# Optimization experiments

Hardware: AMD Instinct MI355X
Metric: run time of the kernel (lower is better)

## Reference

```python
import jax, jax.numpy as jnp
import numpy as np

F = 1024
K = 32
N = 2048
EPS = 1e-6


def setup_inputs() -> dict:
    key = jax.random.key(0)
    ks = jax.random.split(key, 10)
    x = jax.random.normal(ks[0], (N, F), dtype=jnp.float32)
    idx = jax.random.randint(ks[1], (F, K), 0, F)
    norm_w = jnp.ones((F,), dtype=jnp.float32)
    w1 = jax.random.normal(ks[2], (F, K), dtype=jnp.float32) / np.sqrt(K)
    b1 = jnp.zeros((F,), dtype=jnp.float32)
    w2 = jax.random.normal(ks[3], (F, K), dtype=jnp.float32) / np.sqrt(K)
    b2 = jnp.zeros((F,), dtype=jnp.float32)
    amp = jnp.ones((F,), dtype=jnp.float32)
    freq = jnp.ones((F,), dtype=jnp.float32)
    decay = jnp.full((F,), 0.01, dtype=jnp.float32)
    alpha = jnp.ones((1,), dtype=jnp.float32)
    return {"x": x, "in_index_per_out": idx, "norm_w": norm_w,
            "w1": w1, "b1": b1, "amp": amp, "freq": freq, "decay": decay,
            "w2": w2, "b2": b2, "alpha": alpha}


def _rmsnorm(x, g):
    ms = jnp.mean(x * x, axis=-1, keepdims=True)
    return x * jax.lax.rsqrt(ms + EPS) * g


def _geo_sparse_linear(h, idx, w, b):
    hg = h[:, idx]
    return jnp.einsum('nok,ok->no', hg, w) + b


def _sine_param(z, amp, freq, decay):
    return amp * jnp.sin(freq * z) * jnp.exp(-decay * z * z)


def reference(x, in_index_per_out, norm_w, w1, b1, amp, freq, decay, w2, b2, alpha):
    h = _rmsnorm(x, norm_w)
    h = _sine_param(_geo_sparse_linear(h, in_index_per_out, w1, b1), amp, freq, decay)
    h = _geo_sparse_linear(h, in_index_per_out, w2, b2)
    return x + alpha * h
```

## Files before the change

### kernel.cpp

```cpp
#include <hip/hip_runtime.h>
#include <hip/hip_bf16.h>

#define FDIM 1024
#define KNZ 32
#define NROWS 2048
#define RB 8
#define TPB 1024
#define EPSV 1e-6f

static_assert(TPB == FDIM, "o = tid mapping requires TPB == FDIM");
static_assert(NROWS % RB == 0, "rows divide");

__device__ __forceinline__ unsigned int swz(unsigned int i) {
  return i ^ ((i >> 3) & 7u);
}

__device__ __forceinline__ unsigned int f2bf(float f) {
  unsigned int u = __float_as_uint(f);
  u += 0x7fffu + ((u >> 16) & 1u);
  return u >> 16;
}

__device__ __forceinline__ unsigned int pack2bf(float a, float b) {
  return f2bf(a) | (f2bf(b) << 16);
}

__global__ void geo_prep(const int* __restrict__ idx,
                         const float* __restrict__ w1,
                         const float* __restrict__ w2,
                         unsigned* __restrict__ pr1, unsigned* __restrict__ pr2) {
  __shared__ int   li[16 * 33];
  __shared__ float l1[16 * 33];
  __shared__ float l2[16 * 33];
  const int t = threadIdx.x;
  const int o0 = blockIdx.x * 16;
  #pragma unroll
  for (int e = 0; e < 2; ++e) {
    int j = t + e * 256;
    int ol = j >> 5, k = j & 31;
    int g = o0 * KNZ + j;
    li[ol * 33 + k] = idx[g];
    l1[ol * 33 + k] = w1[g];
    l2[ol * 33 + k] = w2[g];
  }
  __syncthreads();
  #pragma unroll
  for (int e = 0; e < 2; ++e) {
    int j = t + e * 256;
    int ol = j & 15, k = j >> 4;
    unsigned off = swz((unsigned)li[ol * 33 + k]);
    unsigned wb1 = __float_as_uint(l1[ol * 33 + k]) & 0xFFFFFC00u;
    unsigned wb2 = __float_as_uint(l2[ol * 33 + k]) & 0xFFFFFC00u;
    pr1[k * FDIM + o0 + ol] = wb1 | off;
    pr2[k * FDIM + o0 + ol] = wb2 | off;
  }
}

__device__ __forceinline__ void gather8(unsigned pw, const uint4* lds, float* acc) {
  float w = __uint_as_float(pw);
  uint4 hv = lds[pw & 1023u];
  const unsigned int* hd = reinterpret_cast<const unsigned int*>(&hv);
  #pragma unroll
  for (int d = 0; d < 4; ++d) {
    acc[2 * d]     = fmaf(__uint_as_float(hd[d] << 16), w, acc[2 * d]);
    acc[2 * d + 1] = fmaf(__uint_as_float(hd[d] & 0xffff0000u), w, acc[2 * d + 1]);
  }
}

template <bool TR>
__global__ __launch_bounds__(TPB, 4)
void geo_main(const float* __restrict__ x, const float* __restrict__ norm_w,
              const float* __restrict__ b1, const float* __restrict__ amp,
              const float* __restrict__ freq, const float* __restrict__ decay,
              const float* __restrict__ b2, const float* __restrict__ alpha,
              const unsigned* __restrict__ pr1, const unsigned* __restrict__ pr2,
              const int* __restrict__ idx, const float* __restrict__ w1,
              const float* __restrict__ w2, float* __restrict__ out) {
  __shared__ uint4 h_lds[FDIM];
  __shared__ uint4 s_lds[FDIM];
  __shared__ float red[(TPB / 64) * RB];
  __shared__ float rs_sh[RB];

  const int tid = threadIdx.x;
  const int lane = tid & 63;
  const int wid = tid >> 6;
  const int r0 = blockIdx.x * RB;
  const int o = tid;

  float v[RB];
  #pragma unroll
  for (int r = 0; r < RB; ++r)
    v[r] = x[(r0 + r) * FDIM + tid];

  const float g = norm_w[tid];

  {
    float p[RB];
    #pragma unroll
    for (int r = 0; r < RB; ++r) p[r] = v[r] * v[r];
    #pragma unroll
    for (int r = 0; r < 4; ++r) {
      float up = __shfl_xor(p[r + 4], 4, 64);
      float dn = __shfl_xor(p[r], 4, 64);
      p[r] = (lane & 4) ? (p[r + 4] + up) : (p[r] + dn);
    }
    #pragma unroll
    for (int r = 0; r < 2; ++r) {
      float up = __shfl_xor(p[r + 2], 2, 64);
      float dn = __shfl_xor(p[r], 2, 64);
      p[r] = (lane & 2) ? (p[r + 2] + up) : (p[r] + dn);
    }
    {
      float up = __shfl_xor(p[1], 1, 64);
      float dn = __shfl_xor(p[0], 1, 64);
      p[0] = (lane & 1) ? (p[1] + up) : (p[0] + dn);
    }
    p[0] += __shfl_xor(p[0], 8, 64);
    p[0] += __shfl_xor(p[0], 16, 64);
    p[0] += __shfl_xor(p[0], 32, 64);
    if (lane < RB) red[wid * RB + lane] = p[0];
  }

  {
    uint4 h;
    h.x = pack2bf(g * v[0], g * v[1]);
    h.y = pack2bf(g * v[2], g * v[3]);
    h.z = pack2bf(g * v[4], g * v[5]);
    h.w = pack2bf(g * v[6], g * v[7]);
    h_lds[swz((unsigned)tid)] = h;
  }

  __syncthreads();

  {
    float a = red[lane] + red[64 + lane];
    a += __shfl_xor(a, 8, 64);
    a += __shfl_xor(a, 16, 64);
    a += __shfl_xor(a, 32, 64);
    if (lane < RB) rs_sh[lane] = rsqrtf(a * (1.0f / FDIM) + EPSV);
  }

  float acc[RB] = {0.f, 0.f, 0.f, 0.f, 0.f, 0.f, 0.f, 0.f};

  if (TR) {
    #pragma unroll
    for (int gk = 0; gk < 4; ++gk) {
      unsigned u[8];
      #pragma unroll
      for (int j = 0; j < 8; ++j) u[j] = pr1[(gk * 8 + j) * FDIM + o];
      #pragma unroll
      for (int j = 0; j < 8; ++j) gather8(u[j], h_lds, acc);
    }
  } else {
    #pragma unroll 8
    for (int k = 0; k < KNZ; ++k) {
      unsigned off = swz((unsigned)idx[o * KNZ + k]);
      unsigned wb = __float_as_uint(w1[o * KNZ + k]) & 0xFFFFFC00u;
      gather8(wb | off, h_lds, acc);
    }
  }

  {
    const float bb1 = b1[o], am = amp[o], fq = freq[o], dc = decay[o];
    const float4 ra = *reinterpret_cast<const float4*>(&rs_sh[0]);
    const float4 rb = *reinterpret_cast<const float4*>(&rs_sh[4]);
    const float rsv[RB] = {ra.x, ra.y, ra.z, ra.w, rb.x, rb.y, rb.z, rb.w};
    float s[RB];
    #pragma unroll
    for (int r = 0; r < RB; ++r) {
      float z = fmaf(acc[r], rsv[r], bb1);
      s[r] = am * __sinf(fq * z) * __expf(-dc * z * z);
    }
    uint4 sv;
    sv.x = pack2bf(s[0], s[1]);
    sv.y = pack2bf(s[2], s[3]);
    sv.z = pack2bf(s[4], s[5]);
    sv.w = pack2bf(s[6], s[7]);
    s_lds[swz((unsigned)o)] = sv;
  }
  __syncthreads();

  #pragma unroll
  for (int r = 0; r < RB; ++r) acc[r] = 0.f;

  if (TR) {
    #pragma unroll
    for (int gk = 0; gk < 4; ++gk) {
      unsigned u[8];
      #pragma unroll
      for (int j = 0; j < 8; ++j) u[j] = pr2[(gk * 8 + j) * FDIM + o];
      #pragma unroll
      for (int j = 0; j < 8; ++j) gather8(u[j], s_lds, acc);
    }
  } else {
    #pragma unroll 8
    for (int k = 0; k < KNZ; ++k) {
      unsigned off = swz((unsigned)idx[o * KNZ + k]);
      unsigned wb = __float_as_uint(w2[o * KNZ + k]) & 0xFFFFFC00u;
      gather8(wb | off, s_lds, acc);
    }
  }

  {
    const float bb2 = b2[o];
    const float al = alpha[0];
    #pragma unroll
    for (int r = 0; r < RB; ++r)
      out[(r0 + r) * FDIM + o] = fmaf(al, acc[r] + bb2, v[r]);
  }
}

extern "C" void kernel_launch(void* const* d_in, const int* in_sizes, int n_in,
                              void* d_out, int out_size, void* d_ws, size_t ws_size,
                              hipStream_t stream) {
  const float* x      = (const float*)d_in[0];
  const int*   idx    = (const int*)d_in[1];
  const float* norm_w = (const float*)d_in[2];
  const float* w1     = (const float*)d_in[3];
  const float* b1     = (const float*)d_in[4];
  const float* amp    = (const float*)d_in[5];
  const float* freq   = (const float*)d_in[6];
  const float* decay  = (const float*)d_in[7];
  const float* w2     = (const float*)d_in[8];
  const float* b2     = (const float*)d_in[9];
  const float* alpha  = (const float*)d_in[10];
  float* out = (float*)d_out;

  const size_t need = 2ull * FDIM * KNZ * sizeof(unsigned);
  if (ws_size >= need) {
    unsigned* pr1 = (unsigned*)d_ws;
    unsigned* pr2 = pr1 + (size_t)FDIM * KNZ;
    geo_prep<<<FDIM / 16, 256, 0, stream>>>(idx, w1, w2, pr1, pr2);
    geo_main<true><<<NROWS / RB, TPB, 0, stream>>>(
        x, norm_w, b1, amp, freq, decay, b2, alpha, pr1, pr2, idx, w1, w2, out);
  } else {
    geo_main<false><<<NROWS / RB, TPB, 0, stream>>>(
        x, norm_w, b1, amp, freq, decay, b2, alpha, nullptr, nullptr, idx, w1, w2, out);
  }
}
```

Before: 21.89 us.

## Switch gathers to packed fp16 FMA and reorder fan-in to spread LDS banks

The activations, weights and accumulators in the sparse gather loops change from bf16 inputs with fp32 FMAs to fp16 with packed half2 FMAs, halving the arithmetic instruction count. The prep kernel now reorders each output's K entries so consecutive steps cycle through different swizzle groups, aiming to cut LDS bank conflicts during the gathers. x is reloaded at the residual instead of being held in registers, which lowers register pressure. Accumulating 32 terms in fp16 loses accuracy and risks overflow, and the prep kernel becomes a serial per-thread loop with only 16 blocks of 64 threads.

```diff
diff --git a/kernel.cpp b/kernel.cpp
--- a/kernel.cpp
+++ b/kernel.cpp
@@ -1,5 +1,5 @@
 #include <hip/hip_runtime.h>
-#include <hip/hip_bf16.h>
+#include <hip/hip_fp16.h>
 
 #define FDIM 1024
 #define KNZ 32
@@ -15,55 +15,69 @@
   return i ^ ((i >> 3) & 7u);
 }
 
-__device__ __forceinline__ unsigned int f2bf(float f) {
-  unsigned int u = __float_as_uint(f);
-  u += 0x7fffu + ((u >> 16) & 1u);
-  return u >> 16;
-}
-
-__device__ __forceinline__ unsigned int pack2bf(float a, float b) {
-  return f2bf(a) | (f2bf(b) << 16);
+__device__ __forceinline__ unsigned f16bits(float f) {
+  return (unsigned)__half_as_ushort(__float2half(f));
 }
 
 __global__ void geo_prep(const int* __restrict__ idx,
                          const float* __restrict__ w1,
                          const float* __restrict__ w2,
                          unsigned* __restrict__ pr1, unsigned* __restrict__ pr2) {
-  __shared__ int   li[16 * 33];
-  __shared__ float l1[16 * 33];
-  __shared__ float l2[16 * 33];
+  __shared__ unsigned short kord[64][33];
+  __shared__ int cnt[64][9];
+  __shared__ int ptr[64][9];
+  __shared__ int rem[64][9];
   const int t = threadIdx.x;
-  const int o0 = blockIdx.x * 16;
-  #pragma unroll
-  for (int e = 0; e < 2; ++e) {
-    int j = t + e * 256;
-    int ol = j >> 5, k = j & 31;
-    int g = o0 * KNZ + j;
-    li[ol * 33 + k] = idx[g];
-    l1[ol * 33 + k] = w1[g];
-    l2[ol * 33 + k] = w2[g];
-  }
-  __syncthreads();
-  #pragma unroll
-  for (int e = 0; e < 2; ++e) {
-    int j = t + e * 256;
-    int ol = j & 15, k = j >> 4;
-    unsigned off = swz((unsigned)li[ol * 33 + k]);
-    unsigned wb1 = __float_as_uint(l1[ol * 33 + k]) & 0xFFFFFC00u;
-    unsigned wb2 = __float_as_uint(l2[ol * 33 + k]) & 0xFFFFFC00u;
-    pr1[k * FDIM + o0 + ol] = wb1 | off;
-    pr2[k * FDIM + o0 + ol] = wb2 | off;
-  }
-}
-
-__device__ __forceinline__ void gather8(unsigned pw, const uint4* lds, float* acc) {
-  float w = __uint_as_float(pw);
-  uint4 hv = lds[pw & 1023u];
-  const unsigned int* hd = reinterpret_cast<const unsigned int*>(&hv);
+  const int o = blockIdx.x * 64 + t;
+
+  #pragma unroll
+  for (int q = 0; q < 8; ++q) cnt[t][q] = 0;
+
+  #pragma unroll
+  for (int k = 0; k < KNZ; ++k) {
+    unsigned off = swz((unsigned)idx[o * KNZ + k]);
+    ++cnt[t][off & 7u];
+  }
+  {
+    int s = 0;
+    #pragma unroll
+    for (int q = 0; q < 8; ++q) { ptr[t][q] = s; s += cnt[t][q]; }
+  }
+  #pragma unroll
+  for (int k = 0; k < KNZ; ++k) {
+    unsigned off = swz((unsigned)idx[o * KNZ + k]);
+    kord[t][ptr[t][off & 7u]++] = (unsigned short)k;
+  }
+  {
+    int s = 0;
+    #pragma unroll
+    for (int q = 0; q < 8; ++q) {
+      int c = cnt[t][q];
+      ptr[t][q] = s; rem[t][q] = c; s += c;
+    }
+  }
+  int qq = t & 7;
+  for (int j = 0; j < KNZ; ++j) {
+    while (rem[t][qq] == 0) qq = (qq + 1) & 7;
+    int k = kord[t][ptr[t][qq]++];
+    --rem[t][qq];
+    qq = (qq + 1) & 7;
+    unsigned off = swz((unsigned)idx[o * KNZ + k]);
+    pr1[j * FDIM + o] = (f16bits(w1[o * KNZ + k]) << 16) | off;
+    pr2[j * FDIM + o] = (f16bits(w2[o * KNZ + k]) << 16) | off;
+  }
+}
+
+__device__ __forceinline__ void gatherh(unsigned e, const uint4* lds,
+                                        __half2* acc2) {
+  unsigned wd = (e & 0xFFFF0000u) | (e >> 16);
+  __half2 w = *reinterpret_cast<__half2*>(&wd);
+  uint4 hv = lds[e & 1023u];
+  const unsigned* hd = reinterpret_cast<const unsigned*>(&hv);
   #pragma unroll
   for (int d = 0; d < 4; ++d) {
-    acc[2 * d]     = fmaf(__uint_as_float(hd[d] << 16), w, acc[2 * d]);
-    acc[2 * d + 1] = fmaf(__uint_as_float(hd[d] & 0xffff0000u), w, acc[2 * d + 1]);
+    __half2 h2 = *reinterpret_cast<const __half2*>(&hd[d]);
+    acc2[d] = __hfma2(h2, w, acc2[d]);
   }
 }
 
@@ -87,14 +101,14 @@
   const int r0 = blockIdx.x * RB;
   const int o = tid;
 
-  float v[RB];
-  #pragma unroll
-  for (int r = 0; r < RB; ++r)
-    v[r] = x[(r0 + r) * FDIM + tid];
-
-  const float g = norm_w[tid];
-
-  {
+  {
+    float v[RB];
+    #pragma unroll
+    for (int r = 0; r < RB; ++r)
+      v[r] = x[(r0 + r) * FDIM + tid];
+
+    const float g = norm_w[tid];
+
     float p[RB];
     #pragma unroll
     for (int r = 0; r < RB; ++r) p[r] = v[r] * v[r];
@@ -119,14 +133,16 @@
     p[0] += __shfl_xor(p[0], 16, 64);
     p[0] += __shfl_xor(p[0], 32, 64);
     if (lane < RB) red[wid * RB + lane] = p[0];
-  }
-
-  {
+
     uint4 h;
-    h.x = pack2bf(g * v[0], g * v[1]);
-    h.y = pack2bf(g * v[2], g * v[3]);
-    h.z = pack2bf(g * v[4], g * v[5]);
-    h.w = pack2bf(g * v[6], g * v[7]);
+    __half2 h01 = __floats2half2_rn(g * v[0], g * v[1]);
+    __half2 h23 = __floats2half2_rn(g * v[2], g * v[3]);
+    __half2 h45 = __floats2half2_rn(g * v[4], g * v[5]);
+    __half2 h67 = __floats2half2_rn(g * v[6], g * v[7]);
+    h.x = *reinterpret_cast<unsigned*>(&h01);
+    h.y = *reinterpret_cast<unsigned*>(&h23);
+    h.z = *reinterpret_cast<unsigned*>(&h45);
+    h.w = *reinterpret_cast<unsigned*>(&h67);
     h_lds[swz((unsigned)tid)] = h;
   }
 
@@ -140,7 +156,12 @@
     if (lane < RB) rs_sh[lane] = rsqrtf(a * (1.0f / FDIM) + EPSV);
   }
 
-  float acc[RB] = {0.f, 0.f, 0.f, 0.f, 0.f, 0.f, 0.f, 0.f};
+  __half2 acc2[4];
+  {
+    unsigned z = 0;
+    #pragma unroll
+    for (int d = 0; d < 4; ++d) acc2[d] = *reinterpret_cast<__half2*>(&z);
+  }
 
   if (TR) {
     #pragma unroll
@@ -149,14 +170,14 @@
       #pragma unroll
       for (int j = 0; j < 8; ++j) u[j] = pr1[(gk * 8 + j) * FDIM + o];
       #pragma unroll
-      for (int j = 0; j < 8; ++j) gather8(u[j], h_lds, acc);
+      for (int j = 0; j < 8; ++j) gatherh(u[j], h_lds, acc2);
     }
   } else {
     #pragma unroll 8
     for (int k = 0; k < KNZ; ++k) {
       unsigned off = swz((unsigned)idx[o * KNZ + k]);
-      unsigned wb = __float_as_uint(w1[o * KNZ + k]) & 0xFFFFFC00u;
-      gather8(wb | off, h_lds, acc);
+      unsigned e = (f16bits(w1[o * KNZ + k]) << 16) | off;
+      gatherh(e, h_lds, acc2);
     }
   }
 
@@ -165,23 +186,36 @@
     const float4 ra = *reinterpret_cast<const float4*>(&rs_sh[0]);
     const float4 rb = *reinterpret_cast<const float4*>(&rs_sh[4]);
     const float rsv[RB] = {ra.x, ra.y, ra.z, ra.w, rb.x, rb.y, rb.z, rb.w};
+    float accf[RB];
+    #pragma unroll
+    for (int d = 0; d < 4; ++d) {
+      float2 f = __half22float2(acc2[d]);
+      accf[2 * d] = f.x; accf[2 * d + 1] = f.y;
+    }
     float s[RB];
     #pragma unroll
     for (int r = 0; r < RB; ++r) {
-      float z = fmaf(acc[r], rsv[r], bb1);
+      float z = fmaf(accf[r], rsv[r], bb1);
       s[r] = am * __sinf(fq * z) * __expf(-dc * z * z);
     }
     uint4 sv;
-    sv.x = pack2bf(s[0], s[1]);
-    sv.y = pack2bf(s[2], s[3]);
-    sv.z = pack2bf(s[4], s[5]);
-    sv.w = pack2bf(s[6], s[7]);
+    __half2 s01 = __floats2half2_rn(s[0], s[1]);
+    __half2 s23 = __floats2half2_rn(s[2], s[3]);
+    __half2 s45 = __floats2half2_rn(s[4], s[5]);
+    __half2 s67 = __floats2half2_rn(s[6], s[7]);
+    sv.x = *reinterpret_cast<unsigned*>(&s01);
+    sv.y = *reinterpret_cast<unsigned*>(&s23);
+    sv.z = *reinterpret_cast<unsigned*>(&s45);
+    sv.w = *reinterpret_cast<unsigned*>(&s67);
     s_lds[swz((unsigned)o)] = sv;
   }
   __syncthreads();
 
-  #pragma unroll
-  for (int r = 0; r < RB; ++r) acc[r] = 0.f;
+  {
+    unsigned z = 0;
+    #pragma unroll
+    for (int d = 0; d < 4; ++d) acc2[d] = *reinterpret_cast<__half2*>(&z);
+  }
 
   if (TR) {
     #pragma unroll
@@ -190,23 +224,30 @@
       #pragma unroll
       for (int j = 0; j < 8; ++j) u[j] = pr2[(gk * 8 + j) * FDIM + o];
       #pragma unroll
-      for (int j = 0; j < 8; ++j) gather8(u[j], s_lds, acc);
+      for (int j = 0; j < 8; ++j) gatherh(u[j], s_lds, acc2);
     }
   } else {
     #pragma unroll 8
     for (int k = 0; k < KNZ; ++k) {
       unsigned off = swz((unsigned)idx[o * KNZ + k]);
-      unsigned wb = __float_as_uint(w2[o * KNZ + k]) & 0xFFFFFC00u;
-      gather8(wb | off, s_lds, acc);
+      unsigned e = (f16bits(w2[o * KNZ + k]) << 16) | off;
+      gatherh(e, s_lds, acc2);
     }
   }
 
   {
     const float bb2 = b2[o];
     const float al = alpha[0];
+    float accf[RB];
+    #pragma unroll
+    for (int d = 0; d < 4; ++d) {
+      float2 f = __half22float2(acc2[d]);
+      accf[2 * d] = f.x; accf[2 * d + 1] = f.y;
+    }
     #pragma unroll
     for (int r = 0; r < RB; ++r)
-      out[(r0 + r) * FDIM + o] = fmaf(al, acc[r] + bb2, v[r]);
+      out[(r0 + r) * FDIM + o] =
+          fmaf(al, accf[r] + bb2, x[(r0 + r) * FDIM + o]);
   }
 }
 
@@ -230,7 +271,7 @@
   if (ws_size >= need) {
     unsigned* pr1 = (unsigned*)d_ws;
     unsigned* pr2 = pr1 + (size_t)FDIM * KNZ;
-    geo_prep<<<FDIM / 16, 256, 0, stream>>>(idx, w1, w2, pr1, pr2);
+    geo_prep<<<FDIM / 64, 64, 0, stream>>>(idx, w1, w2, pr1, pr2);
     geo_main<true><<<NROWS / RB, TPB, 0, stream>>>(
         x, norm_w, b1, amp, freq, decay, b2, alpha, pr1, pr2, idx, w1, w2, out);
   } else {
```

After: 31.90 us. 45.7% more time.
